# Kernel optimization log

Hardware: AMD Instinct MI355X
Metric: run time of the kernel (lower is better)

Reference implementation:

```python
import jax, jax.numpy as jnp
import numpy as np
import math

NUM_ADCS = 64      # P
NUM_SENSORS = 256  # M
NUM_BLOCKS = 32    # B
BATCH = 4096


def setup_inputs() -> dict:
    key = jax.random.key(0)
    k1, k2 = jax.random.split(key)
    x = jax.random.normal(k1, (BATCH, 2 * NUM_SENSORS * NUM_BLOCKS), dtype=jnp.float32)
    p_values = jax.random.normal(k2, (NUM_ADCS, 1), dtype=jnp.float32)
    return {"x": x, "p_values": p_values}


def reference(x, p_values):
    P, M, B = NUM_ADCS, NUM_SENSORS, NUM_BLOCKS
    m = jnp.arange(M, dtype=x.dtype)                 # [M]
    phi = p_values * m                               # [P, M]
    ang = -phi * (2.0 * math.pi / M)
    A_real = jnp.cos(ang)                            # [P, M]
    A_imag = jnp.sin(ang)                            # [P, M]
    A1 = jnp.concatenate((A_real, A_imag), axis=0)   # [2P, M]
    A2 = jnp.concatenate((-A_imag, A_real), axis=0)  # [2P, M]
    A = jnp.concatenate((A1, A2), axis=1)            # [2P, 2M]
    # block_diag(*[A]*B) @ x.T  ==  per-block matmul on reshaped x
    batch = x.shape[0]
    xb = x.reshape(batch, B, 2 * M)                  # [batch, B, 2M]
    yb = jnp.einsum('pm,bnm->bnp', A, xb)            # [batch, B, 2P]
    return yb.reshape(batch, B * 2 * P)
```

## Files before the change

### kernel.cpp

```cpp
#include <hip/hip_runtime.h>
#include <hip/hip_bf16.h>

#define P_ADC 64
#define M_SEN 256
#define B_BLK 32
#define BATCHN 4096

#define GK 512
#define GN 128
#define GR (BATCHN * B_BLK)

typedef float  f32x4  __attribute__((ext_vector_type(4)));
typedef __bf16 bf16x8 __attribute__((ext_vector_type(8)));

__global__ void build_w_frags(const float* __restrict__ pv, __bf16* __restrict__ wfrag) {
    int tid = blockIdx.x * blockDim.x + threadIdx.x;
    if (tid >= 16 * 8 * 64) return;
    int lane = tid & 63;
    int f    = (tid >> 6) & 7;
    int t    = tid >> 9;
    int n    = f * 16 + (lane & 15);
    int g    = lane >> 4;
    int q    = n & 63;
    bool ph  = (n >= 64);
    float pq = pv[q];
    const float step = -0.02454369260617025967f;
    bf16x8 v;
#pragma unroll
    for (int j = 0; j < 8; ++j) {
        int k  = t * 32 + ((j >> 2) << 4) + g * 4 + (j & 3);
        int mm = k & 255;
        bool mh = (k >= 256);
        float ang = pq * (float)mm * step;
        float s, c;
        sincosf(ang, &s, &c);
        float a = (ph == mh) ? c : (ph ? s : -s);
        v[j] = (__bf16)a;
    }
    *(bf16x8*)(wfrag + (size_t)tid * 8) = v;
}

__global__ __launch_bounds__(1024) void analog_gemm(const float* __restrict__ X,
                                                    const __bf16* __restrict__ W,
                                                    float* __restrict__ out) {
    __shared__ __bf16 lw[16 * 8 * 64 * 8];

    const int tid = threadIdx.x;

    {
        const f32x4* src = (const f32x4*)W;
        f32x4* dst = (f32x4*)lw;
#pragma unroll
        for (int i = 0; i < 8; ++i)
            dst[i * 1024 + tid] = src[i * 1024 + tid];
    }
    __syncthreads();

    const int lane = tid & 63;
    const int wave = tid >> 6;
    const int lr = lane & 15;
    const int g  = lane >> 4;

    const bf16x8* wp = (const bf16x8*)lw + lane;

#pragma unroll
    for (int s = 0; s < 2; ++s) {
        const long rowbase = (long)blockIdx.x * 512 + (long)s * 256 + (long)wave * 16;
        const float* xp = X + (rowbase + lr) * (long)GK + g * 4;

        f32x4 acc[8];
#pragma unroll
        for (int f = 0; f < 8; ++f) acc[f] = (f32x4)0.0f;

#pragma unroll
        for (int t = 0; t < 16; ++t) {
            f32x4 xa = *(const f32x4*)(xp + t * 32);
            f32x4 xb = *(const f32x4*)(xp + t * 32 + 16);

            bf16x8 b;
#pragma unroll
            for (int j = 0; j < 4; ++j) {
                b[j]     = (__bf16)xa[j];
                b[4 + j] = (__bf16)xb[j];
            }

#pragma unroll
            for (int f = 0; f < 8; ++f) {
                bf16x8 w = wp[(t * 8 + f) * 64];
                acc[f] = __builtin_amdgcn_mfma_f32_16x16x32_bf16(w, b, acc[f], 0, 0, 0);
            }
        }

        float* op = out + (rowbase + lr) * (long)GN + g * 4;
#pragma unroll
        for (int f = 0; f < 8; ++f)
            __builtin_nontemporal_store(acc[f], (f32x4*)(op + f * 16));
    }
}

extern "C" void kernel_launch(void* const* d_in, const int* in_sizes, int n_in,
                              void* d_out, int out_size, void* d_ws, size_t ws_size,
                              hipStream_t stream) {
    const float* x  = (const float*)d_in[0];
    const float* pv = (const float*)d_in[1];
    float* out      = (float*)d_out;
    __bf16* wfrag   = (__bf16*)d_ws;

    hipLaunchKernelGGL(build_w_frags, dim3(32), dim3(256), 0, stream, pv, wfrag);
    hipLaunchKernelGGL(analog_gemm, dim3(256), dim3(1024), 0, stream, x, wfrag, out);
}
```

Baseline: 72.20 us.

## Exploit block structure of A to halve weight storage and split waves over output halves

The weight matrix [[C,-S],[S,C]]-style structure is exploited: only the first-half-K fragments are built, and the second half of K reuses them with swapped output halves and a sign flip applied to the x operand via XOR on bf16 sign bits. Each pair of waves now shares 16 rows and splits the 128 outputs into two halves, so each wave does half the MFMAs per row group. The grid grows to 1024 blocks of 128 rows each, and LDS use per block is halved, with launch bounds hinting more occupancy. The cost is that each x row is loaded twice (once per wave of the pair), adding redundant global reads in a kernel likely bound by memory bandwidth.

```diff
diff --git a/kernel.cpp b/kernel.cpp
--- a/kernel.cpp
+++ b/kernel.cpp
@@ -12,10 +12,11 @@
 
 typedef float  f32x4  __attribute__((ext_vector_type(4)));
 typedef __bf16 bf16x8 __attribute__((ext_vector_type(8)));
+typedef unsigned int u32x4 __attribute__((ext_vector_type(4)));
 
 __global__ void build_w_frags(const float* __restrict__ pv, __bf16* __restrict__ wfrag) {
     int tid = blockIdx.x * blockDim.x + threadIdx.x;
-    if (tid >= 16 * 8 * 64) return;
+    if (tid >= 8 * 8 * 64) return;
     int lane = tid & 63;
     int f    = (tid >> 6) & 7;
     int t    = tid >> 9;
@@ -29,21 +30,19 @@
 #pragma unroll
     for (int j = 0; j < 8; ++j) {
         int k  = t * 32 + ((j >> 2) << 4) + g * 4 + (j & 3);
-        int mm = k & 255;
-        bool mh = (k >= 256);
-        float ang = pq * (float)mm * step;
+        float ang = pq * (float)k * step;
         float s, c;
         sincosf(ang, &s, &c);
-        float a = (ph == mh) ? c : (ph ? s : -s);
+        float a = ph ? s : c;
         v[j] = (__bf16)a;
     }
     *(bf16x8*)(wfrag + (size_t)tid * 8) = v;
 }
 
-__global__ __launch_bounds__(1024) void analog_gemm(const float* __restrict__ X,
-                                                    const __bf16* __restrict__ W,
-                                                    float* __restrict__ out) {
-    __shared__ __bf16 lw[16 * 8 * 64 * 8];
+__global__ __launch_bounds__(1024, 8) void analog_gemm(const float* __restrict__ X,
+                                                       const __bf16* __restrict__ W,
+                                                       float* __restrict__ out) {
+    __shared__ __bf16 lw[8 * 8 * 64 * 8];
 
     const int tid = threadIdx.x;
 
@@ -51,51 +50,67 @@
         const f32x4* src = (const f32x4*)W;
         f32x4* dst = (f32x4*)lw;
 #pragma unroll
-        for (int i = 0; i < 8; ++i)
+        for (int i = 0; i < 4; ++i)
             dst[i * 1024 + tid] = src[i * 1024 + tid];
     }
     __syncthreads();
 
     const int lane = tid & 63;
     const int wave = tid >> 6;
-    const int lr = lane & 15;
-    const int g  = lane >> 4;
+    const int rs   = wave >> 1;
+    const int ch   = wave & 1;
+    const int lr   = lane & 15;
+    const int g    = lane >> 4;
 
+    const long rowbase = (long)blockIdx.x * 128 + (long)rs * 16;
+    const float* xp = X + (rowbase + lr) * (long)GK + g * 4;
     const bf16x8* wp = (const bf16x8*)lw + lane;
 
+    f32x4 acc[4];
 #pragma unroll
-    for (int s = 0; s < 2; ++s) {
-        const long rowbase = (long)blockIdx.x * 512 + (long)s * 256 + (long)wave * 16;
-        const float* xp = X + (rowbase + lr) * (long)GK + g * 4;
+    for (int f = 0; f < 4; ++f) acc[f] = (f32x4)0.0f;
 
-        f32x4 acc[8];
-#pragma unroll
-        for (int f = 0; f < 8; ++f) acc[f] = (f32x4)0.0f;
+    const int fb  = ch * 4;
+    const int fbS = 4 - fb;
 
 #pragma unroll
-        for (int t = 0; t < 16; ++t) {
-            f32x4 xa = *(const f32x4*)(xp + t * 32);
-            f32x4 xb = *(const f32x4*)(xp + t * 32 + 16);
-
-            bf16x8 b;
+    for (int t = 0; t < 8; ++t) {
+        f32x4 xa = *(const f32x4*)(xp + t * 32);
+        f32x4 xb = *(const f32x4*)(xp + t * 32 + 16);
+        bf16x8 b;
 #pragma unroll
-            for (int j = 0; j < 4; ++j) {
-                b[j]     = (__bf16)xa[j];
-                b[4 + j] = (__bf16)xb[j];
-            }
+        for (int j = 0; j < 4; ++j) { b[j] = (__bf16)xa[j]; b[4 + j] = (__bf16)xb[j]; }
+#pragma unroll
+        for (int f = 0; f < 4; ++f) {
+            bf16x8 w = wp[(t * 8 + fb + f) * 64];
+            acc[f] = __builtin_amdgcn_mfma_f32_16x16x32_bf16(w, b, acc[f], 0, 0, 0);
+        }
+    }
 
 #pragma unroll
-            for (int f = 0; f < 8; ++f) {
-                bf16x8 w = wp[(t * 8 + f) * 64];
-                acc[f] = __builtin_amdgcn_mfma_f32_16x16x32_bf16(w, b, acc[f], 0, 0, 0);
-            }
+    for (int t = 8; t < 16; ++t) {
+        f32x4 xa = *(const f32x4*)(xp + t * 32);
+        f32x4 xb = *(const f32x4*)(xp + t * 32 + 16);
+        bf16x8 b;
+#pragma unroll
+        for (int j = 0; j < 4; ++j) { b[j] = (__bf16)xa[j]; b[4 + j] = (__bf16)xb[j]; }
+        if (ch == 0) {
+            u32x4 u = __builtin_bit_cast(u32x4, b);
+#pragma unroll
+            for (int j = 0; j < 4; ++j) u[j] ^= 0x80008000u;
+            b = __builtin_bit_cast(bf16x8, u);
         }
+#pragma unroll
+        for (int f = 0; f < 4; ++f) {
+            bf16x8 w = wp[((t - 8) * 8 + fbS + f) * 64];
+            acc[f] = __builtin_amdgcn_mfma_f32_16x16x32_bf16(w, b, acc[f], 0, 0, 0);
+        }
+    }
 
-        float* op = out + (rowbase + lr) * (long)GN + g * 4;
+    float* op = out + (rowbase + lr) * (long)GN + fb * 16 + g * 4;
 #pragma unroll
-        for (int f = 0; f < 8; ++f)
-            __builtin_nontemporal_store(acc[f], (f32x4*)(op + f * 16));
-    }
+    for (int f = 0; f < 4; ++f)
+        __builtin_nontemporal_store(acc[f], (f32x4*)(op + f * 16));
 }
 
 extern "C" void kernel_launch(void* const* d_in, const int* in_sizes, int n_in,
@@ -106,6 +121,6 @@
     float* out      = (float*)d_out;
     __bf16* wfrag   = (__bf16*)d_ws;
 
-    hipLaunchKernelGGL(build_w_frags, dim3(32), dim3(256), 0, stream, pv, wfrag);
-    hipLaunchKernelGGL(analog_gemm, dim3(256), dim3(1024), 0, stream, x, wfrag, out);
+    hipLaunchKernelGGL(build_w_frags, dim3(16), dim3(256), 0, stream, pv, wfrag);
+    hipLaunchKernelGGL(analog_gemm, dim3(GR / 128), dim3(1024), 0, stream, x, wfrag, out);
 }
```

New measurement: 85.51 us. 1.18x slower.

## Fuse weight build into GEMM, exploit block symmetry, prefetch X in registers

Applied to the files above, without the earlier changes.

Merges the weight-fragment builder into the GEMM kernel, so each block computes a half-size weight tile in LDS using sinpif/cospif. The second half of K reuses that tile with negated activations, which exploits the [[C,-S],[S,C]] structure of the matrix. The kernel now runs many more, smaller blocks (512 threads, 128 rows each) and software-prefetches X six steps ahead with nontemporal loads. The cost is that every block recomputes trig for the weights, which adds redundant ALU work per block.

```diff
diff --git a/kernel.cpp b/kernel.cpp
--- a/kernel.cpp
+++ b/kernel.cpp
@@ -12,90 +12,96 @@
 
 typedef float  f32x4  __attribute__((ext_vector_type(4)));
 typedef __bf16 bf16x8 __attribute__((ext_vector_type(8)));
+typedef unsigned int u32x4 __attribute__((ext_vector_type(4)));
 
-__global__ void build_w_frags(const float* __restrict__ pv, __bf16* __restrict__ wfrag) {
-    int tid = blockIdx.x * blockDim.x + threadIdx.x;
-    if (tid >= 16 * 8 * 64) return;
-    int lane = tid & 63;
-    int f    = (tid >> 6) & 7;
-    int t    = tid >> 9;
-    int n    = f * 16 + (lane & 15);
-    int g    = lane >> 4;
-    int q    = n & 63;
-    bool ph  = (n >= 64);
-    float pq = pv[q];
-    const float step = -0.02454369260617025967f;
-    bf16x8 v;
+__global__ __launch_bounds__(512, 4) void analog_fused(const float* __restrict__ X,
+                                                       const float* __restrict__ pv,
+                                                       float* __restrict__ out) {
+    __shared__ __bf16 lw[8 * 8 * 64 * 8];
+
+    const int tid  = threadIdx.x;
+    const int lane = tid & 63;
+    const int wave = tid >> 6;
+    const int lr   = lane & 15;
+    const int g    = lane >> 4;
+
+    const long rowbase = (long)blockIdx.x * 128 + (long)wave * 16;
+    const float* xp = X + (rowbase + lr) * (long)GK + g * 4;
+
+    f32x4 pxa[6], pxb[6];
 #pragma unroll
-    for (int j = 0; j < 8; ++j) {
-        int k  = t * 32 + ((j >> 2) << 4) + g * 4 + (j & 3);
-        int mm = k & 255;
-        bool mh = (k >= 256);
-        float ang = pq * (float)mm * step;
-        float s, c;
-        sincosf(ang, &s, &c);
-        float a = (ph == mh) ? c : (ph ? s : -s);
-        v[j] = (__bf16)a;
+    for (int t = 0; t < 6; ++t) {
+        pxa[t] = __builtin_nontemporal_load((const f32x4*)(xp + t * 32));
+        pxb[t] = __builtin_nontemporal_load((const f32x4*)(xp + t * 32 + 16));
     }
-    *(bf16x8*)(wfrag + (size_t)tid * 8) = v;
-}
 
-__global__ __launch_bounds__(1024) void analog_gemm(const float* __restrict__ X,
-                                                    const __bf16* __restrict__ W,
-                                                    float* __restrict__ out) {
-    __shared__ __bf16 lw[16 * 8 * 64 * 8];
-
-    const int tid = threadIdx.x;
-
-    {
-        const f32x4* src = (const f32x4*)W;
-        f32x4* dst = (f32x4*)lw;
 #pragma unroll
-        for (int i = 0; i < 8; ++i)
-            dst[i * 1024 + tid] = src[i * 1024 + tid];
+    for (int i = 0; i < 8; ++i) {
+        int slot = i * 512 + tid;
+        int sl = slot & 63, sf = (slot >> 6) & 7, st = slot >> 9;
+        int n  = sf * 16 + (sl & 15);
+        int sg = sl >> 4;
+        float pq = pv[n & 63];
+        bool ph  = (n >= 64);
+        bf16x8 v;
+#pragma unroll
+        for (int j = 0; j < 8; ++j) {
+            int k = st * 32 + ((j >> 2) << 4) + sg * 4 + (j & 3);
+            float arg = pq * (float)k * (-0.0078125f);
+            float a = ph ? sinpif(arg) : cospif(arg);
+            v[j] = (__bf16)a;
+        }
+        *(bf16x8*)(lw + (size_t)slot * 8) = v;
     }
     __syncthreads();
 
-    const int lane = tid & 63;
-    const int wave = tid >> 6;
-    const int lr = lane & 15;
-    const int g  = lane >> 4;
-
     const bf16x8* wp = (const bf16x8*)lw + lane;
 
+    f32x4 acc[8];
 #pragma unroll
-    for (int s = 0; s < 2; ++s) {
-        const long rowbase = (long)blockIdx.x * 512 + (long)s * 256 + (long)wave * 16;
-        const float* xp = X + (rowbase + lr) * (long)GK + g * 4;
-
-        f32x4 acc[8];
-#pragma unroll
-        for (int f = 0; f < 8; ++f) acc[f] = (f32x4)0.0f;
+    for (int f = 0; f < 8; ++f) acc[f] = (f32x4)0.0f;
 
 #pragma unroll
-        for (int t = 0; t < 16; ++t) {
-            f32x4 xa = *(const f32x4*)(xp + t * 32);
-            f32x4 xb = *(const f32x4*)(xp + t * 32 + 16);
+    for (int t = 0; t < 16; ++t) {
+        f32x4 xa = pxa[t % 6];
+        f32x4 xb = pxb[t % 6];
+        if (t + 6 < 16) {
+            pxa[t % 6] = __builtin_nontemporal_load((const f32x4*)(xp + (t + 6) * 32));
+            pxb[t % 6] = __builtin_nontemporal_load((const f32x4*)(xp + (t + 6) * 32 + 16));
+        }
 
-            bf16x8 b;
+        bf16x8 b;
 #pragma unroll
-            for (int j = 0; j < 4; ++j) {
-                b[j]     = (__bf16)xa[j];
-                b[4 + j] = (__bf16)xb[j];
-            }
+        for (int j = 0; j < 4; ++j) { b[j] = (__bf16)xa[j]; b[4 + j] = (__bf16)xb[j]; }
 
+        if (t < 8) {
 #pragma unroll
             for (int f = 0; f < 8; ++f) {
                 bf16x8 w = wp[(t * 8 + f) * 64];
                 acc[f] = __builtin_amdgcn_mfma_f32_16x16x32_bf16(w, b, acc[f], 0, 0, 0);
             }
+        } else {
+            u32x4 u = __builtin_bit_cast(u32x4, b);
+#pragma unroll
+            for (int j = 0; j < 4; ++j) u[j] ^= 0x80008000u;
+            bf16x8 bneg = __builtin_bit_cast(bf16x8, u);
+#pragma unroll
+            for (int f = 0; f < 4; ++f) {
+                bf16x8 w = wp[((t - 8) * 8 + f + 4) * 64];
+                acc[f] = __builtin_amdgcn_mfma_f32_16x16x32_bf16(w, bneg, acc[f], 0, 0, 0);
+            }
+#pragma unroll
+            for (int f = 4; f < 8; ++f) {
+                bf16x8 w = wp[((t - 8) * 8 + f - 4) * 64];
+                acc[f] = __builtin_amdgcn_mfma_f32_16x16x32_bf16(w, b, acc[f], 0, 0, 0);
+            }
         }
+    }
 
-        float* op = out + (rowbase + lr) * (long)GN + g * 4;
+    float* op = out + (rowbase + lr) * (long)GN + g * 4;
 #pragma unroll
-        for (int f = 0; f < 8; ++f)
-            __builtin_nontemporal_store(acc[f], (f32x4*)(op + f * 16));
-    }
+    for (int f = 0; f < 8; ++f)
+        __builtin_nontemporal_store(acc[f], (f32x4*)(op + f * 16));
 }
 
 extern "C" void kernel_launch(void* const* d_in, const int* in_sizes, int n_in,
@@ -104,8 +110,6 @@
     const float* x  = (const float*)d_in[0];
     const float* pv = (const float*)d_in[1];
     float* out      = (float*)d_out;
-    __bf16* wfrag   = (__bf16*)d_ws;
 
-    hipLaunchKernelGGL(build_w_frags, dim3(32), dim3(256), 0, stream, pv, wfrag);
-    hipLaunchKernelGGL(analog_gemm, dim3(256), dim3(1024), 0, stream, x, wfrag, out);
+    hipLaunchKernelGGL(analog_fused, dim3(GR / 128), dim3(512), 0, stream, x, pv, out);
 }
```

Result: slower. 194.6 us (+169.5%).
